# Optimization experiments

Measured on AMD Instinct MI355X. Metric: run time of the kernel, lower is better.

Reference implementation:

```python
import jax, jax.numpy as jnp
import numpy as np


def setup_inputs() -> dict:
    key = jax.random.key(0)
    k1, k2, k3, k4 = jax.random.split(key, 4)
    B, S, E, H, V = 32, 4096, 512, 1024, 50257
    return {
        "decoder_hidden_s_t_1": jax.random.normal(k1, (B, H), dtype=jnp.float32),
        "mems": jax.random.randint(k2, (B, S), 0, V, dtype=jnp.int64),
        "emb_table": jax.random.normal(k3, (V, E), dtype=jnp.float32) * 0.02,
        "W_w": jax.random.normal(k4, (E, H), dtype=jnp.float32) * (1.0 / np.sqrt(H)),
        "W_b": jnp.zeros((E,), dtype=jnp.float32),
    }


def reference(decoder_hidden_s_t_1, mems, emb_table, W_w, W_b):
    # First-call path: build step_mem_embeddings from the memory token ids.
    # mems: [B, S] int -> mems_emb: [B, S, E]  (dropout is identity in eval)
    mems_emb = emb_table[mems]
    # v_t = tanh(W @ h + b): [B, E]
    v_t = jnp.tanh(decoder_hidden_s_t_1 @ W_w.T + W_b)
    # attention scores over memory slots: [B, S]
    scores = jnp.einsum("bse,be->bs", mems_emb, v_t)
    q_t = jax.nn.softmax(scores, axis=1)
    # weighted memory read: [B, 1, E]
    m_t = jnp.einsum("bs,bse->be", q_t, mems_emb)[:, None, :]
    return m_t
```

## Files before the change

kernel.cpp:

```cpp
#include <hip/hip_runtime.h>
#include <cmath>

#define B_ 32
#define S_ 4096
#define E_ 512
#define H_ 1024

__global__ __launch_bounds__(256) void vt_kernel(const float* __restrict__ h,
                                                 const float* __restrict__ W,
                                                 const float* __restrict__ bias,
                                                 float* __restrict__ vt) {
    int wid  = threadIdx.x >> 6;
    int lane = threadIdx.x & 63;
    int out  = blockIdx.x * 4 + wid;
    int b    = out >> 9;
    int e    = out & (E_ - 1);
    const float* hrow = h + b * H_;
    const float* wrow = W + (size_t)e * H_;
    int base = lane * 16;
    float acc = 0.f;
#pragma unroll
    for (int j = 0; j < 4; ++j) {
        float4 hv = *reinterpret_cast<const float4*>(hrow + base + j * 4);
        float4 wv = *reinterpret_cast<const float4*>(wrow + base + j * 4);
        acc += hv.x * wv.x + hv.y * wv.y + hv.z * wv.z + hv.w * wv.w;
    }
#pragma unroll
    for (int off = 32; off > 0; off >>= 1) acc += __shfl_xor(acc, off, 64);
    if (lane == 0) vt[out] = tanhf(acc + bias[e]);
}

__global__ __launch_bounds__(256) void attn_part_kernel(const int* __restrict__ mems,
                                                        const float* __restrict__ emb,
                                                        const float* __restrict__ vt,
                                                        float* __restrict__ partial,
                                                        int nchunk) {
    int b     = blockIdx.x / nchunk;
    int chunk = blockIdx.x % nchunk;
    int wid   = threadIdx.x >> 6;
    int lane  = threadIdx.x & 63;
    int rows_per_block = S_ / nchunk;
    int s0 = chunk * rows_per_block;

    const float* vrow = vt + (size_t)b * E_ + lane * 8;
    float4 v0 = *reinterpret_cast<const float4*>(vrow);
    float4 v1 = *reinterpret_cast<const float4*>(vrow + 4);

    float m = -1e30f, l = 0.f;
    float4 acc0 = {0.f, 0.f, 0.f, 0.f};
    float4 acc1 = {0.f, 0.f, 0.f, 0.f};

    const int* midx = mems + (size_t)b * S_;

    for (int s = s0 + wid; s < s0 + rows_per_block; s += 4) {
        int idx = midx[s];
        const float* row = emb + (size_t)idx * E_ + lane * 8;
        float4 r0 = *reinterpret_cast<const float4*>(row);
        float4 r1 = *reinterpret_cast<const float4*>(row + 4);
        float p = r0.x * v0.x + r0.y * v0.y + r0.z * v0.z + r0.w * v0.w
                + r1.x * v1.x + r1.y * v1.y + r1.z * v1.z + r1.w * v1.w;
#pragma unroll
        for (int off = 32; off > 0; off >>= 1) p += __shfl_xor(p, off, 64);
        float m_new = fmaxf(m, p);
        float corr  = __expf(m - m_new);
        float w     = __expf(p - m_new);
        l = l * corr + w;
        acc0.x = acc0.x * corr + w * r0.x;
        acc0.y = acc0.y * corr + w * r0.y;
        acc0.z = acc0.z * corr + w * r0.z;
        acc0.w = acc0.w * corr + w * r0.w;
        acc1.x = acc1.x * corr + w * r1.x;
        acc1.y = acc1.y * corr + w * r1.y;
        acc1.z = acc1.z * corr + w * r1.z;
        acc1.w = acc1.w * corr + w * r1.w;
        m = m_new;
    }

    __shared__ float s_m[4], s_l[4];
    __shared__ float s_acc[4][E_];
    if (lane == 0) { s_m[wid] = m; s_l[wid] = l; }
    float* dst = &s_acc[wid][lane * 8];
    reinterpret_cast<float4*>(dst)[0] = acc0;
    reinterpret_cast<float4*>(dst)[1] = acc1;
    __syncthreads();

    float mb = fmaxf(fmaxf(s_m[0], s_m[1]), fmaxf(s_m[2], s_m[3]));
    float f0 = __expf(s_m[0] - mb);
    float f1 = __expf(s_m[1] - mb);
    float f2 = __expf(s_m[2] - mb);
    float f3 = __expf(s_m[3] - mb);
    float lb = s_l[0] * f0 + s_l[1] * f1 + s_l[2] * f2 + s_l[3] * f3;

    float* base = partial + (size_t)(b * nchunk + chunk) * (E_ + 2);
    if (threadIdx.x == 0) { base[0] = mb; base[1] = lb; }
    for (int e = threadIdx.x; e < E_; e += 256) {
        base[2 + e] = s_acc[0][e] * f0 + s_acc[1][e] * f1
                    + s_acc[2][e] * f2 + s_acc[3][e] * f3;
    }
}

__global__ __launch_bounds__(256) void combine_kernel(const float* __restrict__ partial,
                                                      float* __restrict__ out,
                                                      int nchunk) {
    int b = blockIdx.x;
    const int P = E_ + 2;
    float m_g = -1e30f;
    for (int c = 0; c < nchunk; ++c)
        m_g = fmaxf(m_g, partial[(size_t)(b * nchunk + c) * P]);
    float L = 0.f;
    for (int c = 0; c < nchunk; ++c) {
        const float* p = partial + (size_t)(b * nchunk + c) * P;
        L += p[1] * __expf(p[0] - m_g);
    }
    float inv = 1.f / L;
    for (int e = threadIdx.x; e < E_; e += 256) {
        float s = 0.f;
        for (int c = 0; c < nchunk; ++c) {
            const float* p = partial + (size_t)(b * nchunk + c) * P;
            s += __expf(p[0] - m_g) * p[2 + e];
        }
        out[(size_t)b * E_ + e] = s * inv;
    }
}

extern "C" void kernel_launch(void* const* d_in, const int* in_sizes, int n_in,
                              void* d_out, int out_size, void* d_ws, size_t ws_size,
                              hipStream_t stream) {
    const float* h    = (const float*)d_in[0];
    const int*   mems = (const int*)d_in[1];
    const float* emb  = (const float*)d_in[2];
    const float* W    = (const float*)d_in[3];
    const float* bias = (const float*)d_in[4];
    float* out = (float*)d_out;

    float* ws = (float*)d_ws;
    float* vt = ws;
    int nchunk = 32;
    while (nchunk > 1 &&
           (size_t)(B_ * E_ + B_ * nchunk * (E_ + 2)) * sizeof(float) > ws_size) {
        nchunk >>= 1;
    }
    float* partial = ws + B_ * E_;

    hipLaunchKernelGGL(vt_kernel, dim3(B_ * E_ / 4), dim3(256), 0, stream,
                       h, W, bias, vt);
    hipLaunchKernelGGL(attn_part_kernel, dim3(B_ * nchunk), dim3(256), 0, stream,
                       mems, emb, vt, partial, nchunk);
    hipLaunchKernelGGL(combine_kernel, dim3(B_), dim3(256), 0, stream,
                       partial, out, nchunk);
}
```

Measured before the change: 77.47 us.

## Process four gathered rows per iteration, double chunks, parallelize combine over E

```diff
diff --git a/kernel.cpp b/kernel.cpp
--- a/kernel.cpp
+++ b/kernel.cpp
@@ -5,6 +5,7 @@
 #define S_ 4096
 #define E_ 512
 #define H_ 1024
+#define NCHUNK 64
 
 __global__ __launch_bounds__(256) void vt_kernel(const float* __restrict__ h,
                                                  const float* __restrict__ W,
@@ -40,7 +41,8 @@
     int wid   = threadIdx.x >> 6;
     int lane  = threadIdx.x & 63;
     int rows_per_block = S_ / nchunk;
-    int s0 = chunk * rows_per_block;
+    int rows_per_wave  = rows_per_block / 4;
+    int s0 = chunk * rows_per_block + wid * rows_per_wave;
 
     const float* vrow = vt + (size_t)b * E_ + lane * 8;
     float4 v0 = *reinterpret_cast<const float4*>(vrow);
@@ -52,27 +54,55 @@
 
     const int* midx = mems + (size_t)b * S_;
 
-    for (int s = s0 + wid; s < s0 + rows_per_block; s += 4) {
-        int idx = midx[s];
-        const float* row = emb + (size_t)idx * E_ + lane * 8;
-        float4 r0 = *reinterpret_cast<const float4*>(row);
-        float4 r1 = *reinterpret_cast<const float4*>(row + 4);
-        float p = r0.x * v0.x + r0.y * v0.y + r0.z * v0.z + r0.w * v0.w
-                + r1.x * v1.x + r1.y * v1.y + r1.z * v1.z + r1.w * v1.w;
+    for (int it = 0; it < rows_per_wave; it += 4) {
+        int s = s0 + it;
+        int4 idx4 = *reinterpret_cast<const int4*>(midx + s);
+        const float* r0p = emb + (size_t)idx4.x * E_ + lane * 8;
+        const float* r1p = emb + (size_t)idx4.y * E_ + lane * 8;
+        const float* r2p = emb + (size_t)idx4.z * E_ + lane * 8;
+        const float* r3p = emb + (size_t)idx4.w * E_ + lane * 8;
+        float4 a0 = *reinterpret_cast<const float4*>(r0p);
+        float4 b0 = *reinterpret_cast<const float4*>(r0p + 4);
+        float4 a1 = *reinterpret_cast<const float4*>(r1p);
+        float4 b1 = *reinterpret_cast<const float4*>(r1p + 4);
+        float4 a2 = *reinterpret_cast<const float4*>(r2p);
+        float4 b2 = *reinterpret_cast<const float4*>(r2p + 4);
+        float4 a3 = *reinterpret_cast<const float4*>(r3p);
+        float4 b3 = *reinterpret_cast<const float4*>(r3p + 4);
+
+        float p0 = a0.x*v0.x + a0.y*v0.y + a0.z*v0.z + a0.w*v0.w
+                 + b0.x*v1.x + b0.y*v1.y + b0.z*v1.z + b0.w*v1.w;
+        float p1 = a1.x*v0.x + a1.y*v0.y + a1.z*v0.z + a1.w*v0.w
+                 + b1.x*v1.x + b1.y*v1.y + b1.z*v1.z + b1.w*v1.w;
+        float p2 = a2.x*v0.x + a2.y*v0.y + a2.z*v0.z + a2.w*v0.w
+                 + b2.x*v1.x + b2.y*v1.y + b2.z*v1.z + b2.w*v1.w;
+        float p3 = a3.x*v0.x + a3.y*v0.y + a3.z*v0.z + a3.w*v0.w
+                 + b3.x*v1.x + b3.y*v1.y + b3.z*v1.z + b3.w*v1.w;
+
 #pragma unroll
-        for (int off = 32; off > 0; off >>= 1) p += __shfl_xor(p, off, 64);
-        float m_new = fmaxf(m, p);
+        for (int off = 32; off > 0; off >>= 1) {
+            p0 += __shfl_xor(p0, off, 64);
+            p1 += __shfl_xor(p1, off, 64);
+            p2 += __shfl_xor(p2, off, 64);
+            p3 += __shfl_xor(p3, off, 64);
+        }
+
+        float pm    = fmaxf(fmaxf(p0, p1), fmaxf(p2, p3));
+        float m_new = fmaxf(m, pm);
         float corr  = __expf(m - m_new);
-        float w     = __expf(p - m_new);
-        l = l * corr + w;
-        acc0.x = acc0.x * corr + w * r0.x;
-        acc0.y = acc0.y * corr + w * r0.y;
-        acc0.z = acc0.z * corr + w * r0.z;
-        acc0.w = acc0.w * corr + w * r0.w;
-        acc1.x = acc1.x * corr + w * r1.x;
-        acc1.y = acc1.y * corr + w * r1.y;
-        acc1.z = acc1.z * corr + w * r1.z;
-        acc1.w = acc1.w * corr + w * r1.w;
+        float w0 = __expf(p0 - m_new);
+        float w1 = __expf(p1 - m_new);
+        float w2 = __expf(p2 - m_new);
+        float w3 = __expf(p3 - m_new);
+        l = l * corr + (w0 + w1) + (w2 + w3);
+        acc0.x = acc0.x * corr + w0*a0.x + w1*a1.x + w2*a2.x + w3*a3.x;
+        acc0.y = acc0.y * corr + w0*a0.y + w1*a1.y + w2*a2.y + w3*a3.y;
+        acc0.z = acc0.z * corr + w0*a0.z + w1*a1.z + w2*a2.z + w3*a3.z;
+        acc0.w = acc0.w * corr + w0*a0.w + w1*a1.w + w2*a2.w + w3*a3.w;
+        acc1.x = acc1.x * corr + w0*b0.x + w1*b1.x + w2*b2.x + w3*b3.x;
+        acc1.y = acc1.y * corr + w0*b0.y + w1*b1.y + w2*b2.y + w3*b3.y;
+        acc1.z = acc1.z * corr + w0*b0.z + w1*b1.z + w2*b2.z + w3*b3.z;
+        acc1.w = acc1.w * corr + w0*b0.w + w1*b1.w + w2*b2.w + w3*b3.w;
         m = m_new;
     }
 
@@ -99,28 +129,24 @@
     }
 }
 
-__global__ __launch_bounds__(256) void combine_kernel(const float* __restrict__ partial,
+__global__ __launch_bounds__(512) void combine_kernel(const float* __restrict__ partial,
                                                       float* __restrict__ out,
                                                       int nchunk) {
     int b = blockIdx.x;
+    int e = threadIdx.x;
     const int P = E_ + 2;
+    const float* base = partial + (size_t)b * nchunk * P;
     float m_g = -1e30f;
     for (int c = 0; c < nchunk; ++c)
-        m_g = fmaxf(m_g, partial[(size_t)(b * nchunk + c) * P]);
-    float L = 0.f;
+        m_g = fmaxf(m_g, base[(size_t)c * P]);
+    float L = 0.f, s = 0.f;
     for (int c = 0; c < nchunk; ++c) {
-        const float* p = partial + (size_t)(b * nchunk + c) * P;
-        L += p[1] * __expf(p[0] - m_g);
+        const float* p = base + (size_t)c * P;
+        float f = __expf(p[0] - m_g);
+        L += p[1] * f;
+        s += f * p[2 + e];
     }
-    float inv = 1.f / L;
-    for (int e = threadIdx.x; e < E_; e += 256) {
-        float s = 0.f;
-        for (int c = 0; c < nchunk; ++c) {
-            const float* p = partial + (size_t)(b * nchunk + c) * P;
-            s += __expf(p[0] - m_g) * p[2 + e];
-        }
-        out[(size_t)b * E_ + e] = s * inv;
-    }
+    out[(size_t)b * E_ + e] = s / L;
 }
 
 extern "C" void kernel_launch(void* const* d_in, const int* in_sizes, int n_in,
@@ -135,7 +161,7 @@
 
     float* ws = (float*)d_ws;
     float* vt = ws;
-    int nchunk = 32;
+    int nchunk = NCHUNK;
     while (nchunk > 1 &&
            (size_t)(B_ * E_ + B_ * nchunk * (E_ + 2)) * sizeof(float) > ws_size) {
         nchunk >>= 1;
@@ -146,6 +172,6 @@
                        h, W, bias, vt);
     hipLaunchKernelGGL(attn_part_kernel, dim3(B_ * nchunk), dim3(256), 0, stream,
                        mems, emb, vt, partial, nchunk);
-    hipLaunchKernelGGL(combine_kernel, dim3(B_), dim3(256), 0, stream,
+    hipLaunchKernelGGL(combine_kernel, dim3(B_), dim3(512), 0, stream,
                        partial, out, nchunk);
 }
```

Result: slower. 82.85 us (+6.9%).

## Replace per-token gather with vocab histogram and dense score/weighted-sum over table

Applied to the files above, without the earlier changes.

```diff
diff --git a/kernel.cpp b/kernel.cpp
--- a/kernel.cpp
+++ b/kernel.cpp
@@ -5,6 +5,10 @@
 #define S_ 4096
 #define E_ 512
 #define H_ 1024
+#define V_ 50257
+#define CHA 128
+#define CHB 197
+#define NBB 256
 
 __global__ __launch_bounds__(256) void vt_kernel(const float* __restrict__ h,
                                                  const float* __restrict__ W,
@@ -30,97 +34,204 @@
     if (lane == 0) vt[out] = tanhf(acc + bias[e]);
 }
 
-__global__ __launch_bounds__(256) void attn_part_kernel(const int* __restrict__ mems,
-                                                        const float* __restrict__ emb,
-                                                        const float* __restrict__ vt,
-                                                        float* __restrict__ partial,
-                                                        int nchunk) {
-    int b     = blockIdx.x / nchunk;
-    int chunk = blockIdx.x % nchunk;
-    int wid   = threadIdx.x >> 6;
-    int lane  = threadIdx.x & 63;
-    int rows_per_block = S_ / nchunk;
-    int s0 = chunk * rows_per_block;
-
-    const float* vrow = vt + (size_t)b * E_ + lane * 8;
-    float4 v0 = *reinterpret_cast<const float4*>(vrow);
-    float4 v1 = *reinterpret_cast<const float4*>(vrow + 4);
-
+__global__ __launch_bounds__(256) void hist_kernel(const int* __restrict__ mems,
+                                                   int* __restrict__ counts) {
+    int i = blockIdx.x * 256 + threadIdx.x;
+    int b = i >> 12;
+    atomicAdd(counts + (size_t)b * V_ + mems[i], 1);
+}
+
+#define DOT4(t, e) ((t).x*(e).x + (t).y*(e).y + (t).z*(e).z + (t).w*(e).w)
+
+__global__ __launch_bounds__(256) void score_kernel(const float* __restrict__ emb,
+                                                    const float* __restrict__ vt,
+                                                    float* __restrict__ scores) {
+    const int tid   = threadIdx.x;
+    const int vbase = blockIdx.x * CHA;
+    const int bh = tid >> 5;
+    const int vh = tid & 31;
+    const int b0 = bh * 4;
+    const int v0 = vh * 4;
+
+    __shared__ float4 s_emb[CHA][16];
+    __shared__ float4 s_vt[32][16];
+
+    float acc[16];
+#pragma unroll
+    for (int i = 0; i < 16; ++i) acc[i] = 0.f;
+
+    for (int kt = 0; kt < E_; kt += 64) {
+        __syncthreads();
+#pragma unroll
+        for (int j = 0; j < 8; ++j) {
+            int f4  = tid + j * 256;
+            int row = f4 >> 4;
+            int c4  = f4 & 15;
+            int grow = vbase + row; if (grow > V_ - 1) grow = V_ - 1;
+            float4 val = *reinterpret_cast<const float4*>(emb + (size_t)grow * E_ + kt + c4 * 4);
+            s_emb[row][c4 ^ ((row >> 2) & 15)] = val;
+        }
+#pragma unroll
+        for (int j = 0; j < 2; ++j) {
+            int f4  = tid + j * 256;
+            int row = f4 >> 4;
+            int c4  = f4 & 15;
+            s_vt[row][c4] = *reinterpret_cast<const float4*>(vt + row * E_ + kt + c4 * 4);
+        }
+        __syncthreads();
+#pragma unroll
+        for (int k4 = 0; k4 < 16; ++k4) {
+            float4 tv0 = s_vt[b0 + 0][k4];
+            float4 tv1 = s_vt[b0 + 1][k4];
+            float4 tv2 = s_vt[b0 + 2][k4];
+            float4 tv3 = s_vt[b0 + 3][k4];
+            float4 e0 = s_emb[v0 + 0][k4 ^ (((v0 + 0) >> 2) & 15)];
+            float4 e1 = s_emb[v0 + 1][k4 ^ (((v0 + 1) >> 2) & 15)];
+            float4 e2 = s_emb[v0 + 2][k4 ^ (((v0 + 2) >> 2) & 15)];
+            float4 e3 = s_emb[v0 + 3][k4 ^ (((v0 + 3) >> 2) & 15)];
+            acc[0]  += DOT4(tv0, e0); acc[1]  += DOT4(tv0, e1);
+            acc[2]  += DOT4(tv0, e2); acc[3]  += DOT4(tv0, e3);
+            acc[4]  += DOT4(tv1, e0); acc[5]  += DOT4(tv1, e1);
+            acc[6]  += DOT4(tv1, e2); acc[7]  += DOT4(tv1, e3);
+            acc[8]  += DOT4(tv2, e0); acc[9]  += DOT4(tv2, e1);
+            acc[10] += DOT4(tv2, e2); acc[11] += DOT4(tv2, e3);
+            acc[12] += DOT4(tv3, e0); acc[13] += DOT4(tv3, e1);
+            acc[14] += DOT4(tv3, e2); acc[15] += DOT4(tv3, e3);
+        }
+    }
+#pragma unroll
+    for (int j = 0; j < 4; ++j) {
+        size_t base = (size_t)(b0 + j) * V_;
+#pragma unroll
+        for (int i = 0; i < 4; ++i) {
+            int v = vbase + v0 + i;
+            if (v < V_) scores[base + v] = acc[j * 4 + i];
+        }
+    }
+}
+
+__global__ __launch_bounds__(256) void reduce1_kernel(const int* __restrict__ counts,
+                                                      const float* __restrict__ scores,
+                                                      float2* __restrict__ mlpart) {
+    int blk = blockIdx.x;
+    int b = blk >> 3, slice = blk & 7;
+    const int per = (V_ + 7) / 8;
+    int beg = slice * per;
+    int end = beg + per; if (end > V_) end = V_;
     float m = -1e30f, l = 0.f;
-    float4 acc0 = {0.f, 0.f, 0.f, 0.f};
-    float4 acc1 = {0.f, 0.f, 0.f, 0.f};
-
-    const int* midx = mems + (size_t)b * S_;
-
-    for (int s = s0 + wid; s < s0 + rows_per_block; s += 4) {
-        int idx = midx[s];
-        const float* row = emb + (size_t)idx * E_ + lane * 8;
-        float4 r0 = *reinterpret_cast<const float4*>(row);
-        float4 r1 = *reinterpret_cast<const float4*>(row + 4);
-        float p = r0.x * v0.x + r0.y * v0.y + r0.z * v0.z + r0.w * v0.w
-                + r1.x * v1.x + r1.y * v1.y + r1.z * v1.z + r1.w * v1.w;
-#pragma unroll
-        for (int off = 32; off > 0; off >>= 1) p += __shfl_xor(p, off, 64);
-        float m_new = fmaxf(m, p);
-        float corr  = __expf(m - m_new);
-        float w     = __expf(p - m_new);
-        l = l * corr + w;
-        acc0.x = acc0.x * corr + w * r0.x;
-        acc0.y = acc0.y * corr + w * r0.y;
-        acc0.z = acc0.z * corr + w * r0.z;
-        acc0.w = acc0.w * corr + w * r0.w;
-        acc1.x = acc1.x * corr + w * r1.x;
-        acc1.y = acc1.y * corr + w * r1.y;
-        acc1.z = acc1.z * corr + w * r1.z;
-        acc1.w = acc1.w * corr + w * r1.w;
-        m = m_new;
-    }
-
-    __shared__ float s_m[4], s_l[4];
-    __shared__ float s_acc[4][E_];
-    if (lane == 0) { s_m[wid] = m; s_l[wid] = l; }
-    float* dst = &s_acc[wid][lane * 8];
-    reinterpret_cast<float4*>(dst)[0] = acc0;
-    reinterpret_cast<float4*>(dst)[1] = acc1;
+    for (int v = beg + threadIdx.x; v < end; v += 256) {
+        int c = counts[(size_t)b * V_ + v];
+        if (c) {
+            float s = scores[(size_t)b * V_ + v];
+            float mn = fmaxf(m, s);
+            l = l * __expf(m - mn) + (float)c * __expf(s - mn);
+            m = mn;
+        }
+    }
+#pragma unroll
+    for (int off = 32; off > 0; off >>= 1) {
+        float m2 = __shfl_xor(m, off, 64);
+        float l2 = __shfl_xor(l, off, 64);
+        float mn = fmaxf(m, m2);
+        l = l * __expf(m - mn) + l2 * __expf(m2 - mn);
+        m = mn;
+    }
+    __shared__ float sm[4], sl[4];
+    if ((threadIdx.x & 63) == 0) { sm[threadIdx.x >> 6] = m; sl[threadIdx.x >> 6] = l; }
     __syncthreads();
-
-    float mb = fmaxf(fmaxf(s_m[0], s_m[1]), fmaxf(s_m[2], s_m[3]));
-    float f0 = __expf(s_m[0] - mb);
-    float f1 = __expf(s_m[1] - mb);
-    float f2 = __expf(s_m[2] - mb);
-    float f3 = __expf(s_m[3] - mb);
-    float lb = s_l[0] * f0 + s_l[1] * f1 + s_l[2] * f2 + s_l[3] * f3;
-
-    float* base = partial + (size_t)(b * nchunk + chunk) * (E_ + 2);
-    if (threadIdx.x == 0) { base[0] = mb; base[1] = lb; }
-    for (int e = threadIdx.x; e < E_; e += 256) {
-        base[2 + e] = s_acc[0][e] * f0 + s_acc[1][e] * f1
-                    + s_acc[2][e] * f2 + s_acc[3][e] * f3;
-    }
-}
-
-__global__ __launch_bounds__(256) void combine_kernel(const float* __restrict__ partial,
-                                                      float* __restrict__ out,
-                                                      int nchunk) {
-    int b = blockIdx.x;
-    const int P = E_ + 2;
-    float m_g = -1e30f;
-    for (int c = 0; c < nchunk; ++c)
-        m_g = fmaxf(m_g, partial[(size_t)(b * nchunk + c) * P]);
-    float L = 0.f;
-    for (int c = 0; c < nchunk; ++c) {
-        const float* p = partial + (size_t)(b * nchunk + c) * P;
-        L += p[1] * __expf(p[0] - m_g);
-    }
-    float inv = 1.f / L;
-    for (int e = threadIdx.x; e < E_; e += 256) {
-        float s = 0.f;
-        for (int c = 0; c < nchunk; ++c) {
-            const float* p = partial + (size_t)(b * nchunk + c) * P;
-            s += __expf(p[0] - m_g) * p[2 + e];
-        }
-        out[(size_t)b * E_ + e] = s * inv;
-    }
+    if (threadIdx.x == 0) {
+        float M = sm[0], L = sl[0];
+        for (int wv = 1; wv < 4; ++wv) {
+            float mn = fmaxf(M, sm[wv]);
+            L = L * __expf(M - mn) + sl[wv] * __expf(sm[wv] - mn);
+            M = mn;
+        }
+        mlpart[b * 8 + slice] = make_float2(M, L);
+    }
+}
+
+__global__ __launch_bounds__(64) void reduce2_kernel(const float2* __restrict__ mlpart,
+                                                     float2* __restrict__ ml) {
+    int b = threadIdx.x;
+    if (b < B_) {
+        float m = -1e30f, l = 0.f;
+        for (int s = 0; s < 8; ++s) {
+            float2 p = mlpart[b * 8 + s];
+            float mn = fmaxf(m, p.x);
+            l = l * __expf(m - mn) + p.y * __expf(p.x - mn);
+            m = mn;
+        }
+        ml[b] = make_float2(m, 1.f / l);
+    }
+}
+
+__global__ __launch_bounds__(512) void wsum_kernel(const float* __restrict__ emb,
+                                                   const int* __restrict__ counts,
+                                                   const float* __restrict__ scores,
+                                                   const float2* __restrict__ ml,
+                                                   float* __restrict__ partial) {
+    int blk  = blockIdx.x;
+    int rbeg = blk * CHB;
+    int rend = rbeg + CHB; if (rend > V_) rend = V_;
+    int e = threadIdx.x;
+
+    __shared__ float s_w[32][36];
+    __shared__ float2 s_ml[32];
+    if (threadIdx.x < 32) s_ml[threadIdx.x] = ml[threadIdx.x];
+
+    float acc[32];
+#pragma unroll
+    for (int b = 0; b < 32; ++b) acc[b] = 0.f;
+
+    for (int vt0 = rbeg; vt0 < rend; vt0 += 32) {
+        __syncthreads();
+        for (int t = e; t < 1024; t += 512) {
+            int b = t >> 5, vi = t & 31;
+            int v = vt0 + vi;
+            float w = 0.f;
+            if (v < rend) {
+                int c = counts[(size_t)b * V_ + v];
+                if (c) w = (float)c * __expf(scores[(size_t)b * V_ + v] - s_ml[b].x) * s_ml[b].y;
+            }
+            s_w[b][vi] = w;
+        }
+        __syncthreads();
+        int nv = rend - vt0; if (nv > 32) nv = 32;
+        int vi = 0;
+        for (; vi + 4 <= nv; vi += 4) {
+            float ev0 = emb[(size_t)(vt0 + vi + 0) * E_ + e];
+            float ev1 = emb[(size_t)(vt0 + vi + 1) * E_ + e];
+            float ev2 = emb[(size_t)(vt0 + vi + 2) * E_ + e];
+            float ev3 = emb[(size_t)(vt0 + vi + 3) * E_ + e];
+#pragma unroll
+            for (int b = 0; b < 32; ++b) {
+                float4 w4 = *reinterpret_cast<const float4*>(&s_w[b][vi]);
+                acc[b] += w4.x * ev0 + w4.y * ev1 + w4.z * ev2 + w4.w * ev3;
+            }
+        }
+        for (; vi < nv; ++vi) {
+            float ev = emb[(size_t)(vt0 + vi) * E_ + e];
+#pragma unroll
+            for (int b = 0; b < 32; ++b) acc[b] += s_w[b][vi] * ev;
+        }
+    }
+#pragma unroll
+    for (int b = 0; b < 32; ++b)
+        partial[((size_t)blk * 32 + b) * E_ + e] = acc[b];
+}
+
+__global__ __launch_bounds__(64) void combine_kernel(const float* __restrict__ partial,
+                                                     float* __restrict__ out) {
+    int b = blockIdx.x >> 3;
+    int e = (blockIdx.x & 7) * 64 + threadIdx.x;
+    float s0 = 0.f, s1 = 0.f, s2 = 0.f, s3 = 0.f;
+    for (int blk = 0; blk < NBB; blk += 4) {
+        s0 += partial[((size_t)(blk + 0) * 32 + b) * E_ + e];
+        s1 += partial[((size_t)(blk + 1) * 32 + b) * E_ + e];
+        s2 += partial[((size_t)(blk + 2) * 32 + b) * E_ + e];
+        s3 += partial[((size_t)(blk + 3) * 32 + b) * E_ + e];
+    }
+    out[(size_t)b * E_ + e] = (s0 + s1) + (s2 + s3);
 }
 
 extern "C" void kernel_launch(void* const* d_in, const int* in_sizes, int n_in,
@@ -134,18 +245,28 @@
     float* out = (float*)d_out;
 
     float* ws = (float*)d_ws;
-    float* vt = ws;
-    int nchunk = 32;
-    while (nchunk > 1 &&
-           (size_t)(B_ * E_ + B_ * nchunk * (E_ + 2)) * sizeof(float) > ws_size) {
-        nchunk >>= 1;
-    }
-    float* partial = ws + B_ * E_;
+    const size_t CNT = (size_t)B_ * V_;
+    float*  vt      = ws;
+    int*    counts  = (int*)(ws + 16384);
+    float*  scores  = ws + 16384 + CNT;
+    float2* mlpart  = (float2*)(ws + 16384 + 2 * CNT);
+    float2* ml      = mlpart + 256;
+    float*  partial = ws + 16384 + 2 * CNT + 512 + 64;
+
+    hipMemsetAsync(counts, 0, CNT * sizeof(int), stream);
 
     hipLaunchKernelGGL(vt_kernel, dim3(B_ * E_ / 4), dim3(256), 0, stream,
                        h, W, bias, vt);
-    hipLaunchKernelGGL(attn_part_kernel, dim3(B_ * nchunk), dim3(256), 0, stream,
-                       mems, emb, vt, partial, nchunk);
-    hipLaunchKernelGGL(combine_kernel, dim3(B_), dim3(256), 0, stream,
-                       partial, out, nchunk);
-}
+    hipLaunchKernelGGL(hist_kernel, dim3(B_ * S_ / 256), dim3(256), 0, stream,
+                       mems, counts);
+    hipLaunchKernelGGL(score_kernel, dim3((V_ + CHA - 1) / CHA), dim3(256), 0, stream,
+                       emb, vt, scores);
+    hipLaunchKernelGGL(reduce1_kernel, dim3(256), dim3(256), 0, stream,
+                       counts, scores, mlpart);
+    hipLaunchKernelGGL(reduce2_kernel, dim3(1), dim3(64), 0, stream,
+                       mlpart, ml);
+    hipLaunchKernelGGL(wsum_kernel, dim3(NBB), dim3(512), 0, stream,
+                       emb, counts, scores, ml, partial);
+    hipLaunchKernelGGL(combine_kernel, dim3(256), dim3(64), 0, stream,
+                       partial, out);
+}
```

After: 225.6 us. +191.2%, slower.
